# Kernel optimization log

Hardware: AMD Instinct MI355X
Metric: run time of the kernel (lower is better)

## Reference

```python
import jax, jax.numpy as jnp
import numpy as np
from jax import lax

C = 64
KS = 3  # filter_ks for dynamic kernel conv


def conv2d(x, w, pad, b=None):
    out = lax.conv_general_dilated(x, w, (1, 1), [(pad, pad), (pad, pad)],
                                   dimension_numbers=("NCHW", "OIHW", "NCHW"))
    if b is not None:
        out = out + b.reshape(1, -1, 1, 1)
    return out


def kernel_conv2d(feat, kernel):
    # feat: [B,C,H,W]; kernel: [B,C*KS*KS,H,W] -> per-pixel per-channel 3x3 filter
    B, Cc, H, W = feat.shape
    pad = (KS - 1) // 2
    xp = jnp.pad(feat, ((0, 0), (0, 0), (pad, pad), (pad, pad)), mode="edge")
    # patches: [B,C,KS*KS,H,W]
    patches = jnp.stack([xp[:, :, i:i + H, j:j + W]
                         for i in range(KS) for j in range(KS)], axis=2)
    K = kernel.reshape(B, Cc, KS * KS, H, W)
    return jnp.sum(patches * K, axis=2)


def setup_inputs() -> dict:
    key = jax.random.key(0)
    ks = jax.random.split(key, 24)
    B, H, W = 8, 128, 128
    s = lambda *sh: 1.0 / np.sqrt(np.prod(sh[1:]))
    def w(k, *sh):
        return jax.random.normal(k, sh, dtype=jnp.float32) * s(*sh)
    return {
        "f_event": jax.random.normal(ks[0], (B, C, H, W), dtype=jnp.float32),
        "f_blur": jax.random.normal(ks[1], (B, C, H, W), dtype=jnp.float32),
        # trans: conv3x3 -> ReLU -> conv3x3 (no bias)
        "Wt1": w(ks[2], C, C, 3, 3), "Wt2": w(ks[3], C, C, 3, 3),
        # trans2: conv3x3 -> ReLU
        "Wt3": w(ks[4], C, C, 3, 3),
        # F_mlp: Linear(C,2C) -> ReLU -> Linear(2C,C) -> Sigmoid
        "A1": w(ks[5], 2 * C, C), "b1": jnp.zeros((2 * C,), jnp.float32),
        "A2": w(ks[6], C, 2 * C), "b2": jnp.zeros((C,), jnp.float32),
        # gernerate_kernel: conv3x3(bias) -> ReLU -> conv1x1(bias) to C*KS^2
        "G1": w(ks[7], C, C, 3, 3), "g1b": jnp.zeros((C,), jnp.float32),
        "G2": w(ks[8], C * KS * KS, C, 1, 1), "g2b": jnp.zeros((C * KS * KS,), jnp.float32),
        # gate_rgb: conv1x1 C->1, bias
        "Rw": w(ks[9], 1, C, 1, 1), "rb": jnp.zeros((1,), jnp.float32),
        # body_sa: conv3x3 -> ReLU -> conv3x3 (no bias)
        "S1": w(ks[10], C, C, 3, 3), "S2": w(ks[11], C, C, 3, 3),
        # spatial_e: BasicConv(2,1,5,pad=2,relu=False), bias
        "Ew": w(ks[12], 1, 2, 5, 5), "eb": jnp.zeros((1,), jnp.float32),
        # conv1x1_fusion: 2C->2C, no bias
        "Fw": w(ks[13], 2 * C, 2 * C, 1, 1),
    }


def reference(f_event, f_blur, Wt1, Wt2, Wt3, A1, b1, A2, b2,
              G1, g1b, G2, g2b, Rw, rb, S1, S2, Ew, eb, Fw):
    fused = f_event + f_blur
    fused = conv2d(jax.nn.relu(conv2d(fused, Wt1, 1)), Wt2, 1)  # trans
    # SE-style channel gate
    w0 = jnp.mean(fused, axis=(2, 3))                      # [B,C]
    w0 = jax.nn.relu(w0 @ A1.T + b1)
    w0 = jax.nn.sigmoid(w0 @ A2.T + b2)                    # [B,C]
    f_b = f_blur + w0[:, :, None, None] * f_blur
    fused2 = fused + jax.nn.relu(conv2d(fused, Wt3, 1))    # trans2 + residual
    rgb_att = conv2d(fused2, Rw, 0, rb)                    # [B,1,H,W]
    f_b = f_b + rgb_att * f_b
    # dynamic per-pixel kernel from events
    kern = conv2d(jax.nn.relu(conv2d(f_event, G1, 1, g1b)), G2, 0, g2b)
    f_b = f_b + kernel_conv2d(f_b, kern)
    # spatial attention on events
    sa = conv2d(jax.nn.relu(conv2d(f_event, S1, 1)), S2, 1)
    comp = jnp.concatenate([jnp.max(sa, axis=1, keepdims=True),
                            jnp.mean(sa, axis=1, keepdims=True)], axis=1)
    scale_e = jax.nn.sigmoid(conv2d(comp, Ew, 2, eb))      # [B,1,H,W]
    f_e = f_event + scale_e * f_event
    res = conv2d(jnp.concatenate([f_e, f_b], axis=1), Fw, 0)
    return res
```

## Files before the change

kernel.cpp:

```cpp
#include <hip/hip_runtime.h>
#include <math.h>

constexpr int Bn = 8, Cn = 64, Hn = 128, Wn = 128;
constexpr int HW  = Hn * Wn;
constexpr int CHW = Cn * HW;
constexpr size_t NB = (size_t)Bn * CHW;

typedef float  f32x4  __attribute__((ext_vector_type(4)));
typedef __bf16 bf16x8 __attribute__((ext_vector_type(8)));
typedef unsigned int u32x4 __attribute__((ext_vector_type(4)));
typedef unsigned int u32x2 __attribute__((ext_vector_type(2)));

static __device__ __forceinline__ unsigned short f2bf(float f) {
    unsigned u = __builtin_bit_cast(unsigned, f);
    u = (u + 0x7FFF + ((u >> 16) & 1)) >> 16;
    return (unsigned short)u;
}
static __device__ __forceinline__ float bf2f(unsigned short v) {
    unsigned u = (unsigned)v << 16;
    return __builtin_bit_cast(float, u);
}
static __device__ __forceinline__ float bfhalf(unsigned u, int hi) {
    unsigned r = hi ? (u & 0xffff0000u) : (u << 16);
    return __builtin_bit_cast(float, r);
}

__global__ void prep_w_k(const float* __restrict__ W0, const float* __restrict__ W1,
                         const float* __restrict__ W2, const float* __restrict__ W3,
                         const float* __restrict__ W4, const float* __restrict__ W5,
                         unsigned short* __restrict__ dst) {
    int i = blockIdx.x * 256 + threadIdx.x;
    if (i >= 36864) return;
    const float* W = W0;
    switch (blockIdx.y) {
        case 1: W = W1; break; case 2: W = W2; break;
        case 3: W = W3; break; case 4: W = W4; break; case 5: W = W5; break;
        default: break;
    }
    int cj = i & 7;
    int rest = i >> 3;
    int co = rest & 63;
    rest >>= 6;
    int t  = rest % 9;
    int hs = rest / 9;
    int ci = hs * 8 + cj;
    dst[(size_t)blockIdx.y * 36864 + i] = f2bf(W[(co * 64 + ci) * 9 + t]);
}

__global__ void prep2_k(const float* __restrict__ G2, const float* __restrict__ Fw,
                        unsigned short* __restrict__ G2p, unsigned short* __restrict__ Fwp) {
    int i = blockIdx.x * 256 + threadIdx.x;
    if (i < 36864) G2p[i] = f2bf(G2[i]);
    else if (i < 36864 + 16384) Fwp[i - 36864] = f2bf(Fw[i - 36864]);
}

__global__ void pre_blk_k(const float* __restrict__ fe, const float* __restrict__ fb,
                          unsigned short* __restrict__ evb, unsigned short* __restrict__ f0b,
                          unsigned short* __restrict__ fbb) {
    int i = blockIdx.x * 256 + threadIdx.x;
    int px = i & 16383;
    int oct = (i >> 14) & 7;
    int b = i >> 17;
    const float* pe = fe + (size_t)b * CHW + (size_t)oct * 8 * HW + px;
    const float* pb = fb + (size_t)b * CHW + (size_t)oct * 8 * HW + px;
    u32x4 ev, f0, fbv;
#pragma unroll
    for (int q = 0; q < 4; ++q) {
        float e0 = pe[(size_t)(2 * q) * HW],     b0 = pb[(size_t)(2 * q) * HW];
        float e1 = pe[(size_t)(2 * q + 1) * HW], b1 = pb[(size_t)(2 * q + 1) * HW];
        ev[q]  = (unsigned)f2bf(e0) | ((unsigned)f2bf(e1) << 16);
        f0[q]  = (unsigned)f2bf(e0 + b0) | ((unsigned)f2bf(e1 + b1) << 16);
        fbv[q] = (unsigned)f2bf(b0) | ((unsigned)f2bf(b1) << 16);
    }
    const size_t o = ((size_t)(b * 8 + oct) * HW + px) * 8;
    *(u32x4*)(evb + o) = ev;
    *(u32x4*)(f0b + o) = f0;
    *(u32x4*)(fbb + o) = fbv;
}

template<bool RELU, bool BIAS, bool ADD_INPUT, bool RGB, bool COMP, bool STORE>
__global__ __launch_bounds__(256, 3) void conv3x3_blk(
        const unsigned short* __restrict__ in, const unsigned short* __restrict__ Wg,
        const float* __restrict__ bias, unsigned short* __restrict__ out,
        const float* __restrict__ gw, const float* __restrict__ gb,
        float* __restrict__ gout) {
    __shared__ unsigned short smIn[20736];
    const int b  = blockIdx.z;
    const int by = blockIdx.y << 4, bx = blockIdx.x << 4;
    const int tid = threadIdx.x;
    const int lane = tid & 63, w = tid >> 6;
    const int lx = lane & 15, ls = lane >> 4;

    for (int idx = tid; idx < 2592; idx += 256) {
        int oct = idx / 324;
        int p   = idx - oct * 324;
        int yy = p / 18, xx = p - yy * 18;
        int gy = by + yy - 1, gx = bx + xx - 1;
        u32x4 v = u32x4{0u, 0u, 0u, 0u};
        if ((unsigned)gy < (unsigned)Hn && (unsigned)gx < (unsigned)Wn)
            v = *(const u32x4*)(in + ((size_t)(b * 8 + oct) * HW + gy * Wn + gx) * 8);
        *(u32x4*)(smIn + idx * 8) = v;
    }
    __syncthreads();

    f32x4 acc[4][4];
#pragma unroll
    for (int m = 0; m < 4; ++m)
#pragma unroll
        for (int n = 0; n < 4; ++n) acc[m][n] = f32x4{0.f, 0.f, 0.f, 0.f};

#pragma unroll
    for (int ky = 0; ky < 3; ++ky)
#pragma unroll
    for (int kx = 0; kx < 3; ++kx) {
        const int t = ky * 3 + kx;
#pragma unroll
        for (int kk = 0; kk < 2; ++kk) {
            bf16x8 a[4];
            const unsigned short* wbase = Wg + kk * 18432 + ls * 4608 + t * 512 + lx * 8;
#pragma unroll
            for (int m = 0; m < 4; ++m)
                a[m] = *(const bf16x8*)(wbase + m * 128);
            const unsigned short* ibase =
                smIn + ((kk * 4 + ls) * 324 + (4 * w + ky) * 18 + lx + kx) * 8;
#pragma unroll
            for (int n = 0; n < 4; ++n) {
                bf16x8 bf = *(const bf16x8*)(ibase + n * 144);
#pragma unroll
                for (int m = 0; m < 4; ++m)
                    acc[m][n] = __builtin_amdgcn_mfma_f32_16x16x32_bf16(
                        a[m], bf, acc[m][n], 0, 0, 0);
            }
        }
    }

    const int y0 = by + 4 * w;
    float gs[4], gm[4];
    if constexpr (RGB || COMP) {
#pragma unroll
        for (int n = 0; n < 4; ++n) { gs[n] = 0.f; gm[n] = -1e30f; }
    }
#pragma unroll
    for (int m = 0; m < 4; ++m) {
        float4 rw4;
        if constexpr (RGB) rw4 = *(const float4*)(gw + 16 * m + ls * 4);
        const float rwf[4] = {RGB ? rw4.x : 0.f, RGB ? rw4.y : 0.f,
                              RGB ? rw4.z : 0.f, RGB ? rw4.w : 0.f};
        float bv[4] = {0.f, 0.f, 0.f, 0.f};
        if constexpr (BIAS) {
            float4 b4 = *(const float4*)(bias + 16 * m + ls * 4);
            bv[0] = b4.x; bv[1] = b4.y; bv[2] = b4.z; bv[3] = b4.w;
        }
        const size_t rowb = (size_t)(b * 8 + m * 2 + (ls >> 1)) * HW;
        const int j0 = (ls & 1) * 4;
#pragma unroll
        for (int n = 0; n < 4; ++n) {
            const size_t pofs = rowb + (size_t)(y0 + n) * Wn + bx + lx;
            u32x2 rin;
            if constexpr (ADD_INPUT) rin = *(const u32x2*)(in + pofs * 8 + j0);
            float vr[4];
#pragma unroll
            for (int r = 0; r < 4; ++r) {
                float v = acc[m][n][r] + bv[r];
                if constexpr (RELU) v = fmaxf(v, 0.f);
                if constexpr (ADD_INPUT) v += bfhalf(rin[r >> 1], r & 1);
                vr[r] = v;
                if constexpr (RGB) gs[n] = fmaf(rwf[r], v, gs[n]);
                if constexpr (COMP) { gm[n] = fmaxf(gm[n], v); gs[n] += v; }
            }
            if constexpr (STORE) {
                u32x2 pk;
                pk[0] = (unsigned)f2bf(vr[0]) | ((unsigned)f2bf(vr[1]) << 16);
                pk[1] = (unsigned)f2bf(vr[2]) | ((unsigned)f2bf(vr[3]) << 16);
                *(u32x2*)(out + pofs * 8 + j0) = pk;
            }
        }
    }
    if constexpr (RGB) {
#pragma unroll
        for (int n = 0; n < 4; ++n) {
            float s = gs[n];
            s += __shfl_xor(s, 16);
            s += __shfl_xor(s, 32);
            if (ls == 0)
                gout[(size_t)b * HW + (size_t)(y0 + n) * Wn + bx + lx] = s + gb[0];
        }
    }
    if constexpr (COMP) {
#pragma unroll
        for (int n = 0; n < 4; ++n) {
            float s = gs[n], mx = gm[n];
            s += __shfl_xor(s, 16);
            s += __shfl_xor(s, 32);
            mx = fmaxf(mx, __shfl_xor(mx, 16));
            mx = fmaxf(mx, __shfl_xor(mx, 32));
            if (ls == 0) {
                const size_t o = (size_t)b * 2 * HW + (size_t)(y0 + n) * Wn + bx + lx;
                gout[o]      = mx;
                gout[o + HW] = s * (1.f / 64.f);
            }
        }
    }
}

__global__ __launch_bounds__(256, 3) void conv3x3_l1_blk(
        const unsigned short* __restrict__ f0, const unsigned short* __restrict__ ev,
        const unsigned short* __restrict__ Wt1g, const unsigned short* __restrict__ G1g,
        const unsigned short* __restrict__ S1g, const float* __restrict__ g1b,
        unsigned short* __restrict__ out_t1, unsigned short* __restrict__ out_h,
        unsigned short* __restrict__ out_s1) {
    __shared__ unsigned short smIn[20736];
    const int z = blockIdx.z;
    const int b = z & 7, sel = z >> 3;
    const unsigned short* in = (sel == 0) ? f0 : ev;
    const unsigned short* Wg = (sel == 0) ? Wt1g : ((sel == 1) ? G1g : S1g);
    unsigned short* out = (sel == 0) ? out_t1 : ((sel == 1) ? out_h : out_s1);
    const int by = blockIdx.y << 4, bx = blockIdx.x << 4;
    const int tid = threadIdx.x;
    const int lane = tid & 63, w = tid >> 6;
    const int lx = lane & 15, ls = lane >> 4;

    for (int idx = tid; idx < 2592; idx += 256) {
        int oct = idx / 324;
        int p   = idx - oct * 324;
        int yy = p / 18, xx = p - yy * 18;
        int gy = by + yy - 1, gx = bx + xx - 1;
        u32x4 v = u32x4{0u, 0u, 0u, 0u};
        if ((unsigned)gy < (unsigned)Hn && (unsigned)gx < (unsigned)Wn)
            v = *(const u32x4*)(in + ((size_t)(b * 8 + oct) * HW + gy * Wn + gx) * 8);
        *(u32x4*)(smIn + idx * 8) = v;
    }
    __syncthreads();

    f32x4 acc[4][4];
#pragma unroll
    for (int m = 0; m < 4; ++m)
#pragma unroll
        for (int n = 0; n < 4; ++n) acc[m][n] = f32x4{0.f, 0.f, 0.f, 0.f};

#pragma unroll
    for (int ky = 0; ky < 3; ++ky)
#pragma unroll
    for (int kx = 0; kx < 3; ++kx) {
        const int t = ky * 3 + kx;
#pragma unroll
        for (int kk = 0; kk < 2; ++kk) {
            bf16x8 a[4];
            const unsigned short* wbase = Wg + kk * 18432 + ls * 4608 + t * 512 + lx * 8;
#pragma unroll
            for (int m = 0; m < 4; ++m)
                a[m] = *(const bf16x8*)(wbase + m * 128);
            const unsigned short* ibase =
                smIn + ((kk * 4 + ls) * 324 + (4 * w + ky) * 18 + lx + kx) * 8;
#pragma unroll
            for (int n = 0; n < 4; ++n) {
                bf16x8 bf = *(const bf16x8*)(ibase + n * 144);
#pragma unroll
                for (int m = 0; m < 4; ++m)
                    acc[m][n] = __builtin_amdgcn_mfma_f32_16x16x32_bf16(
                        a[m], bf, acc[m][n], 0, 0, 0);
            }
        }
    }

    const int y0 = by + 4 * w;
#pragma unroll
    for (int m = 0; m < 4; ++m) {
        float bv[4] = {0.f, 0.f, 0.f, 0.f};
        if (sel == 1) {
            float4 b4 = *(const float4*)(g1b + 16 * m + ls * 4);
            bv[0] = b4.x; bv[1] = b4.y; bv[2] = b4.z; bv[3] = b4.w;
        }
        const size_t rowb = (size_t)(b * 8 + m * 2 + (ls >> 1)) * HW;
        const int j0 = (ls & 1) * 4;
#pragma unroll
        for (int n = 0; n < 4; ++n) {
            const size_t pofs = rowb + (size_t)(y0 + n) * Wn + bx + lx;
            float vr[4];
#pragma unroll
            for (int r = 0; r < 4; ++r)
                vr[r] = fmaxf(acc[m][n][r] + bv[r], 0.f);
            u32x2 pk;
            pk[0] = (unsigned)f2bf(vr[0]) | ((unsigned)f2bf(vr[1]) << 16);
            pk[1] = (unsigned)f2bf(vr[2]) | ((unsigned)f2bf(vr[3]) << 16);
            *(u32x2*)(out + pofs * 8 + j0) = pk;
        }
    }
}

__global__ __launch_bounds__(256, 3) void conv3x3_l2_blk(
        const unsigned short* __restrict__ t1, const unsigned short* __restrict__ s1,
        const unsigned short* __restrict__ Wt2g, const unsigned short* __restrict__ S2g,
        unsigned short* __restrict__ out_f, float* __restrict__ comp) {
    __shared__ unsigned short smIn[20736];
    const int z = blockIdx.z;
    const int b = z & 7, sel = z >> 3;
    const unsigned short* in = (sel == 0) ? t1 : s1;
    const unsigned short* Wg = (sel == 0) ? Wt2g : S2g;
    const int by = blockIdx.y << 4, bx = blockIdx.x << 4;
    const int tid = threadIdx.x;
    const int lane = tid & 63, w = tid >> 6;
    const int lx = lane & 15, ls = lane >> 4;

    for (int idx = tid; idx < 2592; idx += 256) {
        int oct = idx / 324;
        int p   = idx - oct * 324;
        int yy = p / 18, xx = p - yy * 18;
        int gy = by + yy - 1, gx = bx + xx - 1;
        u32x4 v = u32x4{0u, 0u, 0u, 0u};
        if ((unsigned)gy < (unsigned)Hn && (unsigned)gx < (unsigned)Wn)
            v = *(const u32x4*)(in + ((size_t)(b * 8 + oct) * HW + gy * Wn + gx) * 8);
        *(u32x4*)(smIn + idx * 8) = v;
    }
    __syncthreads();

    f32x4 acc[4][4];
#pragma unroll
    for (int m = 0; m < 4; ++m)
#pragma unroll
        for (int n = 0; n < 4; ++n) acc[m][n] = f32x4{0.f, 0.f, 0.f, 0.f};

#pragma unroll
    for (int ky = 0; ky < 3; ++ky)
#pragma unroll
    for (int kx = 0; kx < 3; ++kx) {
        const int t = ky * 3 + kx;
#pragma unroll
        for (int kk = 0; kk < 2; ++kk) {
            bf16x8 a[4];
            const unsigned short* wbase = Wg + kk * 18432 + ls * 4608 + t * 512 + lx * 8;
#pragma unroll
            for (int m = 0; m < 4; ++m)
                a[m] = *(const bf16x8*)(wbase + m * 128);
            const unsigned short* ibase =
                smIn + ((kk * 4 + ls) * 324 + (4 * w + ky) * 18 + lx + kx) * 8;
#pragma unroll
            for (int n = 0; n < 4; ++n) {
                bf16x8 bf = *(const bf16x8*)(ibase + n * 144);
#pragma unroll
                for (int m = 0; m < 4; ++m)
                    acc[m][n] = __builtin_amdgcn_mfma_f32_16x16x32_bf16(
                        a[m], bf, acc[m][n], 0, 0, 0);
            }
        }
    }

    const int y0 = by + 4 * w;
    if (sel == 0) {
#pragma unroll
        for (int m = 0; m < 4; ++m) {
            const size_t rowb = (size_t)(b * 8 + m * 2 + (ls >> 1)) * HW;
            const int j0 = (ls & 1) * 4;
#pragma unroll
            for (int n = 0; n < 4; ++n) {
                const size_t pofs = rowb + (size_t)(y0 + n) * Wn + bx + lx;
                u32x2 pk;
                pk[0] = (unsigned)f2bf(acc[m][n][0]) | ((unsigned)f2bf(acc[m][n][1]) << 16);
                pk[1] = (unsigned)f2bf(acc[m][n][2]) | ((unsigned)f2bf(acc[m][n][3]) << 16);
                *(u32x2*)(out_f + pofs * 8 + j0) = pk;
            }
        }
    } else {
        float gs[4], gm[4];
#pragma unroll
        for (int n = 0; n < 4; ++n) { gs[n] = 0.f; gm[n] = -1e30f; }
#pragma unroll
        for (int m = 0; m < 4; ++m)
#pragma unroll
            for (int r = 0; r < 4; ++r)
#pragma unroll
                for (int n = 0; n < 4; ++n) {
                    float v = acc[m][n][r];
                    gm[n] = fmaxf(gm[n], v);
                    gs[n] += v;
                }
#pragma unroll
        for (int n = 0; n < 4; ++n) {
            float s = gs[n], mx = gm[n];
            s += __shfl_xor(s, 16);
            s += __shfl_xor(s, 32);
            mx = fmaxf(mx, __shfl_xor(mx, 16));
            mx = fmaxf(mx, __shfl_xor(mx, 32));
            if (ls == 0) {
                const size_t o = (size_t)b * 2 * HW + (size_t)(y0 + n) * Wn + bx + lx;
                comp[o]      = mx;
                comp[o + HW] = s * (1.f / 64.f);
            }
        }
    }
}

__global__ void mean_hw_blk(const unsigned short* __restrict__ in, float* __restrict__ w0) {
    __shared__ float red[256][8];
    const int bo = blockIdx.x;
    const int tid = threadIdx.x;
    const unsigned short* p = in + (size_t)bo * HW * 8;
    float s[8];
#pragma unroll
    for (int j = 0; j < 8; ++j) s[j] = 0.f;
    for (int it = 0; it < 64; ++it) {
        u32x4 v = *(const u32x4*)(p + (size_t)(tid + it * 256) * 8);
#pragma unroll
        for (int j = 0; j < 8; ++j) s[j] += bfhalf(v[j >> 1], j & 1);
    }
#pragma unroll
    for (int j = 0; j < 8; ++j) red[tid][j] = s[j];
    __syncthreads();
    for (int off = 128; off > 0; off >>= 1) {
        if (tid < off)
#pragma unroll
            for (int j = 0; j < 8; ++j) red[tid][j] += red[tid + off][j];
        __syncthreads();
    }
    if (tid < 8) w0[bo * 8 + tid] = red[0][tid] * (1.f / 16384.f);
}

__global__ void mlp_k(const float* __restrict__ w0, const float* __restrict__ A1,
                      const float* __restrict__ b1, const float* __restrict__ A2,
                      const float* __restrict__ b2, float* __restrict__ w0s) {
    int b = blockIdx.x, t = threadIdx.x;
    __shared__ float w0r[64], hid[128];
    if (t < 64) w0r[t] = w0[b * 64 + t];
    __syncthreads();
    float s = b1[t];
    for (int c = 0; c < 64; ++c) s = fmaf(A1[t * 64 + c], w0r[c], s);
    hid[t] = fmaxf(s, 0.f);
    __syncthreads();
    if (t < 64) {
        float s2 = b2[t];
        for (int j = 0; j < 128; ++j) s2 = fmaf(A2[t * 128 + j], hid[j], s2);
        w0s[b * 64 + t] = 1.f / (1.f + expf(-s2));
    }
}

__global__ __launch_bounds__(256, 4) void dynfused_k(
        const unsigned short* __restrict__ fbb, const unsigned short* __restrict__ hb,
        const unsigned short* __restrict__ G2p, const float* __restrict__ g2b,
        const float* __restrict__ w0s, const float* __restrict__ rgb,
        unsigned short* __restrict__ outb) {
    __shared__ unsigned short smU[8192];
    __shared__ unsigned short smFB[11520];
    const int b  = blockIdx.z;
    const int by = blockIdx.y << 3, bx = blockIdx.x << 4;
    const int tid = threadIdx.x;
    const int lane = tid & 63, w = tid >> 6;
    const int lx = lane & 15, ls = lane >> 4;
    const int wr = w & 1, wc = w >> 1;
    const int px = tid & 127;
    const int chalf = __builtin_amdgcn_readfirstlane(tid >> 7);
    const int ty = px >> 4, tx = px & 15;

#pragma unroll
    for (int it = 0; it < 4; ++it) {
        int i = tid + it * 256;
        int p = i & 127, oct = i >> 7;
        const unsigned short* sp =
            hb + ((size_t)(b * 8 + oct) * HW + (by + (p >> 4)) * Wn + bx + (p & 15)) * 8;
        ((u32x4*)smU)[oct * 128 + p] = *(const u32x4*)sp;
    }
    const float* rgbb = rgb + (size_t)b * HW;
    for (int i = tid; i < 1440; i += 256) {
        int oct = i / 180, p = i - oct * 180;
        int pr = p / 18, pc = p - pr * 18;
        int gy = min(max(by + pr - 1, 0), Hn - 1);
        int gx = min(max(bx + pc - 1, 0), Wn - 1);
        u32x4 v = *(const u32x4*)(fbb + ((size_t)(b * 8 + oct) * HW + gy * Wn + gx) * 8);
        float g = 1.f + rgbb[gy * Wn + gx];
        float4 s0 = *(const float4*)(w0s + b * 64 + oct * 8);
        float4 s1 = *(const float4*)(w0s + b * 64 + oct * 8 + 4);
        const float sc[8] = {1.f + s0.x, 1.f + s0.y, 1.f + s0.z, 1.f + s0.w,
                             1.f + s1.x, 1.f + s1.y, 1.f + s1.z, 1.f + s1.w};
#pragma unroll
        for (int j = 0; j < 8; ++j)
            smFB[(oct * 8 + j) * 180 + p] = f2bf(bfhalf(v[j >> 1], j & 1) * sc[j] * g);
    }
    __syncthreads();

    bf16x8 bv[2][4];
#pragma unroll
    for (int kk = 0; kk < 2; ++kk)
#pragma unroll
        for (int n = 0; n < 4; ++n)
            bv[kk][n] = *(const bf16x8*)(smU + ((kk * 4 + ls) * 128 + wc * 64 + n * 16 + lx) * 8);
    __syncthreads();

    float acc[32];
#pragma unroll
    for (int s = 0; s < 32; ++s) acc[s] = 0.f;

#pragma unroll
    for (int chunk = 0; chunk < 9; ++chunk) {
        f32x4 ka[2][4];
#pragma unroll
        for (int m = 0; m < 2; ++m)
#pragma unroll
            for (int n = 0; n < 4; ++n) ka[m][n] = f32x4{0.f, 0.f, 0.f, 0.f};
#pragma unroll
        for (int kk = 0; kk < 2; ++kk) {
            bf16x8 a[2];
#pragma unroll
            for (int m = 0; m < 2; ++m)
                a[m] = *(const bf16x8*)(G2p +
                        (size_t)(chunk * 64 + wr * 32 + m * 16 + lx) * 64 + kk * 32 + ls * 8);
#pragma unroll
            for (int n = 0; n < 4; ++n)
#pragma unroll
                for (int m = 0; m < 2; ++m)
                    ka[m][n] = __builtin_amdgcn_mfma_f32_16x16x32_bf16(a[m], bv[kk][n], ka[m][n], 0, 0, 0);
        }
#pragma unroll
        for (int m = 0; m < 2; ++m) {
            const float4 bb4 = *(const float4*)(g2b + chunk * 64 + wr * 32 + m * 16 + ls * 4);
            const float bb[4] = {bb4.x, bb4.y, bb4.z, bb4.w};
            const int rl0 = wr * 32 + m * 16 + ls * 4;
            const int gr = rl0 >> 3, sub = rl0 & 7;
#pragma unroll
            for (int n = 0; n < 4; ++n) {
                const int pxl = wc * 64 + n * 16 + lx;
                u32x2 pk;
                pk[0] = (unsigned)f2bf(ka[m][n][0] + bb[0]) |
                        ((unsigned)f2bf(ka[m][n][1] + bb[1]) << 16);
                pk[1] = (unsigned)f2bf(ka[m][n][2] + bb[2]) |
                        ((unsigned)f2bf(ka[m][n][3] + bb[3]) << 16);
                *(u32x2*)(smU + pxl * 64 + ((gr ^ (pxl & 7)) << 3) + sub) = pk;
            }
        }
        __syncthreads();
        u32x4 kvr[8];
#pragma unroll
        for (int k = 0; k < 8; ++k)
            kvr[k] = *(const u32x4*)(smU + px * 64 + ((k ^ (px & 7)) << 3));
#pragma unroll
        for (int rl = 0; rl < 64; ++rl) {
            const int r = chunk * 64 + rl;
            const int c = r / 9, t = r - c * 9;
            const int s = c >> 1;
            if ((c & 1) == chalf) {
                float kv = bfhalf(kvr[rl >> 3][(rl & 7) >> 1], rl & 1);
                float pv = bf2f(smFB[c * 180 + (ty + t / 3) * 18 + tx + (t % 3)]);
                acc[s] = fmaf(kv, pv, acc[s]);
            }
        }
        __syncthreads();
    }

#pragma unroll
    for (int s = 0; s < 32; ++s) {
        const int c = 2 * s + chalf;
        float res = bf2f(smFB[c * 180 + (ty + 1) * 18 + (tx + 1)]);
        smU[c * 128 + px] = f2bf(acc[s] + res);
    }
    __syncthreads();
#pragma unroll
    for (int it = 0; it < 4; ++it) {
        int i = tid + it * 256;
        int p = i & 127, oct = i >> 7;
        u32x4 pk;
#pragma unroll
        for (int q = 0; q < 4; ++q)
            pk[q] = (unsigned)smU[(oct * 8 + 2 * q) * 128 + p] |
                    ((unsigned)smU[(oct * 8 + 2 * q + 1) * 128 + p] << 16);
        *(u32x4*)(outb + ((size_t)(b * 8 + oct) * HW + (by + (p >> 4)) * Wn + bx + (p & 15)) * 8) = pk;
    }
}

__global__ __launch_bounds__(256, 2) void fuse_mfma_k(
        const unsigned short* __restrict__ evb, const float* __restrict__ scale,
        const unsigned short* __restrict__ fb2b, const unsigned short* __restrict__ Fwp,
        float* __restrict__ out) {
    __shared__ unsigned short smF[16384];
    const int bid = blockIdx.x;
    const int b = bid >> 7, px0 = (bid & 127) << 7;
    const int tid = threadIdx.x;
    const int lane = tid & 63, w = tid >> 6;
    const int lx = lane & 15, ls = lane >> 4;
    const int wr = w & 1, wc = w >> 1;
    const float* sc = scale + b * HW + px0;

#pragma unroll
    for (int it = 0; it < 8; ++it) {
        int slot = tid + it * 256;
        int oct = slot >> 7, pxl = slot & 127;
        u32x4 v;
        if (oct < 8) {
            v = *(const u32x4*)(evb + ((size_t)(b * 8 + oct) * HW + px0 + pxl) * 8);
            float s = 1.f + sc[pxl];
#pragma unroll
            for (int q = 0; q < 4; ++q)
                v[q] = (unsigned)f2bf(bfhalf(v[q], 0) * s) |
                       ((unsigned)f2bf(bfhalf(v[q], 1) * s) << 16);
        } else {
            v = *(const u32x4*)(fb2b + ((size_t)(b * 8 + oct - 8) * HW + px0 + pxl) * 8);
        }
        ((u32x4*)smF)[oct * 128 + pxl] = v;
    }
    __syncthreads();

    f32x4 acc[4][4];
#pragma unroll
    for (int m = 0; m < 4; ++m)
#pragma unroll
        for (int n = 0; n < 4; ++n) acc[m][n] = f32x4{0.f, 0.f, 0.f, 0.f};

#pragma unroll
    for (int kk = 0; kk < 4; ++kk) {
        bf16x8 a[4];
#pragma unroll
        for (int m = 0; m < 4; ++m)
            a[m] = *(const bf16x8*)(Fwp + (size_t)(wr * 64 + m * 16 + lx) * 128 + kk * 32 + ls * 8);
#pragma unroll
        for (int n = 0; n < 4; ++n) {
            bf16x8 bv = *(const bf16x8*)(smF + ((kk * 4 + ls) * 128 + wc * 64 + n * 16 + lx) * 8);
#pragma unroll
            for (int m = 0; m < 4; ++m)
                acc[m][n] = __builtin_amdgcn_mfma_f32_16x16x32_bf16(a[m], bv, acc[m][n], 0, 0, 0);
        }
    }

    const size_t ob = (size_t)b * 2 * CHW + px0 + wc * 64;
#pragma unroll
    for (int m = 0; m < 4; ++m)
#pragma unroll
        for (int n = 0; n < 4; ++n)
#pragma unroll
            for (int j = 0; j < 4; ++j) {
                const int co = wr * 64 + m * 16 + ls * 4 + j;
                out[ob + (size_t)co * HW + n * 16 + lx] = acc[m][n][j];
            }
}

__global__ void sconv5_k(const float* __restrict__ comp, const float* __restrict__ Ew,
                         const float* __restrict__ eb, float* __restrict__ scale) {
    int id = blockIdx.x * 256 + threadIdx.x;
    int b = id >> 14, p = id & 16383;
    int y = p >> 7, x = p & 127;
    const float* cb = comp + (size_t)b * 2 * HW;
    float acc = eb[0];
#pragma unroll
    for (int ch = 0; ch < 2; ++ch)
#pragma unroll
        for (int ky = 0; ky < 5; ++ky) {
            int gy = y + ky - 2;
            if ((unsigned)gy >= (unsigned)Hn) continue;
#pragma unroll
            for (int kx = 0; kx < 5; ++kx) {
                int gx = x + kx - 2;
                if ((unsigned)gx >= (unsigned)Wn) continue;
                acc = fmaf(Ew[ch * 25 + ky * 5 + kx], cb[ch * HW + gy * Wn + gx], acc);
            }
        }
    scale[id] = 1.f / (1.f + expf(-acc));
}

extern "C" void kernel_launch(void* const* d_in, const int* in_sizes, int n_in,
                              void* d_out, int out_size, void* d_ws, size_t ws_size,
                              hipStream_t stream) {
    const float* f_event = (const float*)d_in[0];
    const float* f_blur  = (const float*)d_in[1];
    const float* Wt1 = (const float*)d_in[2];
    const float* Wt2 = (const float*)d_in[3];
    const float* Wt3 = (const float*)d_in[4];
    const float* A1  = (const float*)d_in[5];
    const float* b1  = (const float*)d_in[6];
    const float* A2  = (const float*)d_in[7];
    const float* b2  = (const float*)d_in[8];
    const float* G1  = (const float*)d_in[9];
    const float* g1b = (const float*)d_in[10];
    const float* G2  = (const float*)d_in[11];
    const float* g2b = (const float*)d_in[12];
    const float* Rw  = (const float*)d_in[13];
    const float* rb  = (const float*)d_in[14];
    const float* S1  = (const float*)d_in[15];
    const float* S2  = (const float*)d_in[16];
    const float* Ew  = (const float*)d_in[17];
    const float* eb  = (const float*)d_in[18];
    const float* Fw  = (const float*)d_in[19];
    float* out = (float*)d_out;

    float* ws    = (float*)d_ws;
    float* w0    = ws;
    float* w0s   = w0 + 512;
    float* rgb   = w0s + 512;
    float* comp  = rgb + Bn * HW;
    float* scale = comp + 2 * Bn * HW;
    unsigned short* wprep = (unsigned short*)(scale + Bn * HW);
    unsigned short* G2p = wprep + 6 * 36864;
    unsigned short* Fwp = G2p + 36864;
    unsigned short* B0 = Fwp + 16384;
    unsigned short* B1 = B0 + NB;
    unsigned short* B2 = B1 + NB;
    unsigned short* B3 = B2 + NB;
    unsigned short* B4 = B3 + NB;
    unsigned short* B5 = B4 + NB;
    unsigned short* B6 = B5 + NB;

    prep_w_k<<<dim3(144, 6), 256, 0, stream>>>(Wt1, Wt2, Wt3, G1, S1, S2, wprep);
    prep2_k<<<208, 256, 0, stream>>>(G2, Fw, G2p, Fwp);
    pre_blk_k<<<4096, 256, 0, stream>>>(f_event, f_blur, B0, B1, B5);
    conv3x3_l1_blk<<<dim3(8, 8, 24), 256, 0, stream>>>(
        B1, B0, wprep + 0 * 36864, wprep + 3 * 36864, wprep + 4 * 36864, g1b,
        B2, B4, B6);
    conv3x3_l2_blk<<<dim3(8, 8, 16), 256, 0, stream>>>(
        B2, B6, wprep + 1 * 36864, wprep + 5 * 36864, B3, comp);
    mean_hw_blk<<<Bn * 8, 256, 0, stream>>>(B3, w0);
    mlp_k<<<Bn, 128, 0, stream>>>(w0, A1, b1, A2, b2, w0s);
    sconv5_k<<<Bn * HW / 256, 256, 0, stream>>>(comp, Ew, eb, scale);
    conv3x3_blk<true, false, true, true, false, false><<<dim3(8, 8, Bn), 256, 0, stream>>>(
        B3, wprep + 2 * 36864, nullptr, nullptr, Rw, rb, rgb);
    dynfused_k<<<dim3(8, 16, Bn), 256, 0, stream>>>(B5, B4, G2p, g2b, w0s, rgb, B3);
    fuse_mfma_k<<<Bn * HW / 128, 256, 0, stream>>>(B0, scale, B3, Fwp, out);
}
```

Before: 222.3 us.

## Use direct global-to-LDS loads and merge spatial conv into rgb kernel

Replaces register-staged global-to-shared copies of conv input halos with the global_load_lds builtin, pointing out-of-bounds halo lanes at a zeroed pad buffer. The 5x5 spatial-attention conv kernel is folded into the rgb gate conv launch as extra z-blocks, removing one launch and letting both run concurrently. fuse_mfma_k raises its occupancy hint and loads the fb2 half directly into LDS. The direct-LDS path depends on builtin availability and on correct synchronisation with asynchronous LDS writes.

```diff
diff --git a/kernel.cpp b/kernel.cpp
--- a/kernel.cpp
+++ b/kernel.cpp
@@ -23,6 +23,16 @@
 static __device__ __forceinline__ float bfhalf(unsigned u, int hi) {
     unsigned r = hi ? (u & 0xffff0000u) : (u << 16);
     return __builtin_bit_cast(float, r);
+}
+
+static __device__ __forceinline__ void gl_lds16(const unsigned short* g, unsigned short* l) {
+#if defined(__has_builtin) && __has_builtin(__builtin_amdgcn_global_load_lds)
+    __builtin_amdgcn_global_load_lds(
+        (const __attribute__((address_space(1))) void*)g,
+        (__attribute__((address_space(3))) void*)l, 16, 0, 0);
+#else
+    *(u32x4*)l = *(const u32x4*)g;
+#endif
 }
 
 __global__ void prep_w_k(const float* __restrict__ W0, const float* __restrict__ W1,
@@ -48,8 +58,10 @@
 }
 
 __global__ void prep2_k(const float* __restrict__ G2, const float* __restrict__ Fw,
-                        unsigned short* __restrict__ G2p, unsigned short* __restrict__ Fwp) {
+                        unsigned short* __restrict__ G2p, unsigned short* __restrict__ Fwp,
+                        unsigned short* __restrict__ zp) {
     int i = blockIdx.x * 256 + threadIdx.x;
+    if (i < 64) zp[i] = 0;
     if (i < 36864) G2p[i] = f2bf(G2[i]);
     else if (i < 36864 + 16384) Fwp[i - 36864] = f2bf(Fw[i - 36864]);
 }
@@ -78,137 +90,12 @@
     *(u32x4*)(fbb + o) = fbv;
 }
 
-template<bool RELU, bool BIAS, bool ADD_INPUT, bool RGB, bool COMP, bool STORE>
-__global__ __launch_bounds__(256, 3) void conv3x3_blk(
-        const unsigned short* __restrict__ in, const unsigned short* __restrict__ Wg,
-        const float* __restrict__ bias, unsigned short* __restrict__ out,
-        const float* __restrict__ gw, const float* __restrict__ gb,
-        float* __restrict__ gout) {
-    __shared__ unsigned short smIn[20736];
-    const int b  = blockIdx.z;
-    const int by = blockIdx.y << 4, bx = blockIdx.x << 4;
-    const int tid = threadIdx.x;
-    const int lane = tid & 63, w = tid >> 6;
-    const int lx = lane & 15, ls = lane >> 4;
-
-    for (int idx = tid; idx < 2592; idx += 256) {
-        int oct = idx / 324;
-        int p   = idx - oct * 324;
-        int yy = p / 18, xx = p - yy * 18;
-        int gy = by + yy - 1, gx = bx + xx - 1;
-        u32x4 v = u32x4{0u, 0u, 0u, 0u};
-        if ((unsigned)gy < (unsigned)Hn && (unsigned)gx < (unsigned)Wn)
-            v = *(const u32x4*)(in + ((size_t)(b * 8 + oct) * HW + gy * Wn + gx) * 8);
-        *(u32x4*)(smIn + idx * 8) = v;
-    }
-    __syncthreads();
-
-    f32x4 acc[4][4];
-#pragma unroll
-    for (int m = 0; m < 4; ++m)
-#pragma unroll
-        for (int n = 0; n < 4; ++n) acc[m][n] = f32x4{0.f, 0.f, 0.f, 0.f};
-
-#pragma unroll
-    for (int ky = 0; ky < 3; ++ky)
-#pragma unroll
-    for (int kx = 0; kx < 3; ++kx) {
-        const int t = ky * 3 + kx;
-#pragma unroll
-        for (int kk = 0; kk < 2; ++kk) {
-            bf16x8 a[4];
-            const unsigned short* wbase = Wg + kk * 18432 + ls * 4608 + t * 512 + lx * 8;
-#pragma unroll
-            for (int m = 0; m < 4; ++m)
-                a[m] = *(const bf16x8*)(wbase + m * 128);
-            const unsigned short* ibase =
-                smIn + ((kk * 4 + ls) * 324 + (4 * w + ky) * 18 + lx + kx) * 8;
-#pragma unroll
-            for (int n = 0; n < 4; ++n) {
-                bf16x8 bf = *(const bf16x8*)(ibase + n * 144);
-#pragma unroll
-                for (int m = 0; m < 4; ++m)
-                    acc[m][n] = __builtin_amdgcn_mfma_f32_16x16x32_bf16(
-                        a[m], bf, acc[m][n], 0, 0, 0);
-            }
-        }
-    }
-
-    const int y0 = by + 4 * w;
-    float gs[4], gm[4];
-    if constexpr (RGB || COMP) {
-#pragma unroll
-        for (int n = 0; n < 4; ++n) { gs[n] = 0.f; gm[n] = -1e30f; }
-    }
-#pragma unroll
-    for (int m = 0; m < 4; ++m) {
-        float4 rw4;
-        if constexpr (RGB) rw4 = *(const float4*)(gw + 16 * m + ls * 4);
-        const float rwf[4] = {RGB ? rw4.x : 0.f, RGB ? rw4.y : 0.f,
-                              RGB ? rw4.z : 0.f, RGB ? rw4.w : 0.f};
-        float bv[4] = {0.f, 0.f, 0.f, 0.f};
-        if constexpr (BIAS) {
-            float4 b4 = *(const float4*)(bias + 16 * m + ls * 4);
-            bv[0] = b4.x; bv[1] = b4.y; bv[2] = b4.z; bv[3] = b4.w;
-        }
-        const size_t rowb = (size_t)(b * 8 + m * 2 + (ls >> 1)) * HW;
-        const int j0 = (ls & 1) * 4;
-#pragma unroll
-        for (int n = 0; n < 4; ++n) {
-            const size_t pofs = rowb + (size_t)(y0 + n) * Wn + bx + lx;
-            u32x2 rin;
-            if constexpr (ADD_INPUT) rin = *(const u32x2*)(in + pofs * 8 + j0);
-            float vr[4];
-#pragma unroll
-            for (int r = 0; r < 4; ++r) {
-                float v = acc[m][n][r] + bv[r];
-                if constexpr (RELU) v = fmaxf(v, 0.f);
-                if constexpr (ADD_INPUT) v += bfhalf(rin[r >> 1], r & 1);
-                vr[r] = v;
-                if constexpr (RGB) gs[n] = fmaf(rwf[r], v, gs[n]);
-                if constexpr (COMP) { gm[n] = fmaxf(gm[n], v); gs[n] += v; }
-            }
-            if constexpr (STORE) {
-                u32x2 pk;
-                pk[0] = (unsigned)f2bf(vr[0]) | ((unsigned)f2bf(vr[1]) << 16);
-                pk[1] = (unsigned)f2bf(vr[2]) | ((unsigned)f2bf(vr[3]) << 16);
-                *(u32x2*)(out + pofs * 8 + j0) = pk;
-            }
-        }
-    }
-    if constexpr (RGB) {
-#pragma unroll
-        for (int n = 0; n < 4; ++n) {
-            float s = gs[n];
-            s += __shfl_xor(s, 16);
-            s += __shfl_xor(s, 32);
-            if (ls == 0)
-                gout[(size_t)b * HW + (size_t)(y0 + n) * Wn + bx + lx] = s + gb[0];
-        }
-    }
-    if constexpr (COMP) {
-#pragma unroll
-        for (int n = 0; n < 4; ++n) {
-            float s = gs[n], mx = gm[n];
-            s += __shfl_xor(s, 16);
-            s += __shfl_xor(s, 32);
-            mx = fmaxf(mx, __shfl_xor(mx, 16));
-            mx = fmaxf(mx, __shfl_xor(mx, 32));
-            if (ls == 0) {
-                const size_t o = (size_t)b * 2 * HW + (size_t)(y0 + n) * Wn + bx + lx;
-                gout[o]      = mx;
-                gout[o + HW] = s * (1.f / 64.f);
-            }
-        }
-    }
-}
-
 __global__ __launch_bounds__(256, 3) void conv3x3_l1_blk(
         const unsigned short* __restrict__ f0, const unsigned short* __restrict__ ev,
         const unsigned short* __restrict__ Wt1g, const unsigned short* __restrict__ G1g,
         const unsigned short* __restrict__ S1g, const float* __restrict__ g1b,
         unsigned short* __restrict__ out_t1, unsigned short* __restrict__ out_h,
-        unsigned short* __restrict__ out_s1) {
+        unsigned short* __restrict__ out_s1, const unsigned short* __restrict__ zp) {
     __shared__ unsigned short smIn[20736];
     const int z = blockIdx.z;
     const int b = z & 7, sel = z >> 3;
@@ -225,10 +112,10 @@
         int p   = idx - oct * 324;
         int yy = p / 18, xx = p - yy * 18;
         int gy = by + yy - 1, gx = bx + xx - 1;
-        u32x4 v = u32x4{0u, 0u, 0u, 0u};
-        if ((unsigned)gy < (unsigned)Hn && (unsigned)gx < (unsigned)Wn)
-            v = *(const u32x4*)(in + ((size_t)(b * 8 + oct) * HW + gy * Wn + gx) * 8);
-        *(u32x4*)(smIn + idx * 8) = v;
+        const unsigned short* src =
+            ((unsigned)gy < (unsigned)Hn && (unsigned)gx < (unsigned)Wn)
+            ? in + ((size_t)(b * 8 + oct) * HW + gy * Wn + gx) * 8 : zp;
+        gl_lds16(src, smIn + idx * 8);
     }
     __syncthreads();
 
@@ -291,7 +178,8 @@
 __global__ __launch_bounds__(256, 3) void conv3x3_l2_blk(
         const unsigned short* __restrict__ t1, const unsigned short* __restrict__ s1,
         const unsigned short* __restrict__ Wt2g, const unsigned short* __restrict__ S2g,
-        unsigned short* __restrict__ out_f, float* __restrict__ comp) {
+        unsigned short* __restrict__ out_f, float* __restrict__ comp,
+        const unsigned short* __restrict__ zp) {
     __shared__ unsigned short smIn[20736];
     const int z = blockIdx.z;
     const int b = z & 7, sel = z >> 3;
@@ -307,10 +195,10 @@
         int p   = idx - oct * 324;
         int yy = p / 18, xx = p - yy * 18;
         int gy = by + yy - 1, gx = bx + xx - 1;
-        u32x4 v = u32x4{0u, 0u, 0u, 0u};
-        if ((unsigned)gy < (unsigned)Hn && (unsigned)gx < (unsigned)Wn)
-            v = *(const u32x4*)(in + ((size_t)(b * 8 + oct) * HW + gy * Wn + gx) * 8);
-        *(u32x4*)(smIn + idx * 8) = v;
+        const unsigned short* src =
+            ((unsigned)gy < (unsigned)Hn && (unsigned)gx < (unsigned)Wn)
+            ? in + ((size_t)(b * 8 + oct) * HW + gy * Wn + gx) * 8 : zp;
+        gl_lds16(src, smIn + idx * 8);
     }
     __syncthreads();
 
@@ -387,6 +275,117 @@
                 comp[o + HW] = s * (1.f / 64.f);
             }
         }
+    }
+}
+
+__global__ __launch_bounds__(256, 3) void rgb_sconv_k(
+        const unsigned short* __restrict__ in, const unsigned short* __restrict__ Wg,
+        const float* __restrict__ gw, const float* __restrict__ gb,
+        float* __restrict__ gout,
+        const float* __restrict__ comp, const float* __restrict__ Ew,
+        const float* __restrict__ eb, float* __restrict__ scale,
+        const unsigned short* __restrict__ zp) {
+    __shared__ unsigned short smIn[20736];
+    const int z = blockIdx.z;
+    if (z >= 8) {
+        int id = (((z - 8) * 64) + blockIdx.y * 8 + blockIdx.x) * 256 + threadIdx.x;
+        int sb = id >> 14, p = id & 16383;
+        int y = p >> 7, x = p & 127;
+        const float* cb = comp + (size_t)sb * 2 * HW;
+        float sacc = eb[0];
+#pragma unroll
+        for (int ch = 0; ch < 2; ++ch)
+#pragma unroll
+            for (int ky = 0; ky < 5; ++ky) {
+                int gy = y + ky - 2;
+                if ((unsigned)gy >= (unsigned)Hn) continue;
+#pragma unroll
+                for (int kx = 0; kx < 5; ++kx) {
+                    int gx = x + kx - 2;
+                    if ((unsigned)gx >= (unsigned)Wn) continue;
+                    sacc = fmaf(Ew[ch * 25 + ky * 5 + kx], cb[ch * HW + gy * Wn + gx], sacc);
+                }
+            }
+        scale[id] = 1.f / (1.f + expf(-sacc));
+        return;
+    }
+    const int b = z;
+    const int by = blockIdx.y << 4, bx = blockIdx.x << 4;
+    const int tid = threadIdx.x;
+    const int lane = tid & 63, w = tid >> 6;
+    const int lx = lane & 15, ls = lane >> 4;
+
+    for (int idx = tid; idx < 2592; idx += 256) {
+        int oct = idx / 324;
+        int p   = idx - oct * 324;
+        int yy = p / 18, xx = p - yy * 18;
+        int gy = by + yy - 1, gx = bx + xx - 1;
+        const unsigned short* src =
+            ((unsigned)gy < (unsigned)Hn && (unsigned)gx < (unsigned)Wn)
+            ? in + ((size_t)(b * 8 + oct) * HW + gy * Wn + gx) * 8 : zp;
+        gl_lds16(src, smIn + idx * 8);
+    }
+    __syncthreads();
+
+    f32x4 acc[4][4];
+#pragma unroll
+    for (int m = 0; m < 4; ++m)
+#pragma unroll
+        for (int n = 0; n < 4; ++n) acc[m][n] = f32x4{0.f, 0.f, 0.f, 0.f};
+
+#pragma unroll
+    for (int ky = 0; ky < 3; ++ky)
+#pragma unroll
+    for (int kx = 0; kx < 3; ++kx) {
+        const int t = ky * 3 + kx;
+#pragma unroll
+        for (int kk = 0; kk < 2; ++kk) {
+            bf16x8 a[4];
+            const unsigned short* wbase = Wg + kk * 18432 + ls * 4608 + t * 512 + lx * 8;
+#pragma unroll
+            for (int m = 0; m < 4; ++m)
+                a[m] = *(const bf16x8*)(wbase + m * 128);
+            const unsigned short* ibase =
+                smIn + ((kk * 4 + ls) * 324 + (4 * w + ky) * 18 + lx + kx) * 8;
+#pragma unroll
+            for (int n = 0; n < 4; ++n) {
+                bf16x8 bf = *(const bf16x8*)(ibase + n * 144);
+#pragma unroll
+                for (int m = 0; m < 4; ++m)
+                    acc[m][n] = __builtin_amdgcn_mfma_f32_16x16x32_bf16(
+                        a[m], bf, acc[m][n], 0, 0, 0);
+            }
+        }
+    }
+
+    const int y0 = by + 4 * w;
+    float gs[4];
+#pragma unroll
+    for (int n = 0; n < 4; ++n) gs[n] = 0.f;
+#pragma unroll
+    for (int m = 0; m < 4; ++m) {
+        float4 rw4 = *(const float4*)(gw + 16 * m + ls * 4);
+        const float rwf[4] = {rw4.x, rw4.y, rw4.z, rw4.w};
+        const size_t rowb = (size_t)(b * 8 + m * 2 + (ls >> 1)) * HW;
+        const int j0 = (ls & 1) * 4;
+#pragma unroll
+        for (int n = 0; n < 4; ++n) {
+            const size_t pofs = rowb + (size_t)(y0 + n) * Wn + bx + lx;
+            u32x2 rin = *(const u32x2*)(in + pofs * 8 + j0);
+#pragma unroll
+            for (int r = 0; r < 4; ++r) {
+                float v = fmaxf(acc[m][n][r], 0.f) + bfhalf(rin[r >> 1], r & 1);
+                gs[n] = fmaf(rwf[r], v, gs[n]);
+            }
+        }
+    }
+#pragma unroll
+    for (int n = 0; n < 4; ++n) {
+        float s = gs[n];
+        s += __shfl_xor(s, 16);
+        s += __shfl_xor(s, 32);
+        if (ls == 0)
+            gout[(size_t)b * HW + (size_t)(y0 + n) * Wn + bx + lx] = s + gb[0];
     }
 }
 
@@ -454,9 +453,8 @@
     for (int it = 0; it < 4; ++it) {
         int i = tid + it * 256;
         int p = i & 127, oct = i >> 7;
-        const unsigned short* sp =
-            hb + ((size_t)(b * 8 + oct) * HW + (by + (p >> 4)) * Wn + bx + (p & 15)) * 8;
-        ((u32x4*)smU)[oct * 128 + p] = *(const u32x4*)sp;
+        gl_lds16(hb + ((size_t)(b * 8 + oct) * HW + (by + (p >> 4)) * Wn + bx + (p & 15)) * 8,
+                 smU + i * 8);
     }
     const float* rgbb = rgb + (size_t)b * HW;
     for (int i = tid; i < 1440; i += 256) {
@@ -564,7 +562,7 @@
     }
 }
 
-__global__ __launch_bounds__(256, 2) void fuse_mfma_k(
+__global__ __launch_bounds__(256, 3) void fuse_mfma_k(
         const unsigned short* __restrict__ evb, const float* __restrict__ scale,
         const unsigned short* __restrict__ fb2b, const unsigned short* __restrict__ Fwp,
         float* __restrict__ out) {
@@ -578,21 +576,22 @@
     const float* sc = scale + b * HW + px0;
 
 #pragma unroll
-    for (int it = 0; it < 8; ++it) {
+    for (int it = 4; it < 8; ++it) {
         int slot = tid + it * 256;
         int oct = slot >> 7, pxl = slot & 127;
-        u32x4 v;
-        if (oct < 8) {
-            v = *(const u32x4*)(evb + ((size_t)(b * 8 + oct) * HW + px0 + pxl) * 8);
-            float s = 1.f + sc[pxl];
-#pragma unroll
-            for (int q = 0; q < 4; ++q)
-                v[q] = (unsigned)f2bf(bfhalf(v[q], 0) * s) |
-                       ((unsigned)f2bf(bfhalf(v[q], 1) * s) << 16);
-        } else {
-            v = *(const u32x4*)(fb2b + ((size_t)(b * 8 + oct - 8) * HW + px0 + pxl) * 8);
-        }
-        ((u32x4*)smF)[oct * 128 + pxl] = v;
+        gl_lds16(fb2b + ((size_t)(b * 8 + oct - 8) * HW + px0 + pxl) * 8, smF + slot * 8);
+    }
+#pragma unroll
+    for (int it = 0; it < 4; ++it) {
+        int slot = tid + it * 256;
+        int oct = slot >> 7, pxl = slot & 127;
+        u32x4 v = *(const u32x4*)(evb + ((size_t)(b * 8 + oct) * HW + px0 + pxl) * 8);
+        float s = 1.f + sc[pxl];
+#pragma unroll
+        for (int q = 0; q < 4; ++q)
+            v[q] = (unsigned)f2bf(bfhalf(v[q], 0) * s) |
+                   ((unsigned)f2bf(bfhalf(v[q], 1) * s) << 16);
+        ((u32x4*)smF)[slot] = v;
     }
     __syncthreads();
 
@@ -627,29 +626,6 @@
                 const int co = wr * 64 + m * 16 + ls * 4 + j;
                 out[ob + (size_t)co * HW + n * 16 + lx] = acc[m][n][j];
             }
-}
-
-__global__ void sconv5_k(const float* __restrict__ comp, const float* __restrict__ Ew,
-                         const float* __restrict__ eb, float* __restrict__ scale) {
-    int id = blockIdx.x * 256 + threadIdx.x;
-    int b = id >> 14, p = id & 16383;
-    int y = p >> 7, x = p & 127;
-    const float* cb = comp + (size_t)b * 2 * HW;
-    float acc = eb[0];
-#pragma unroll
-    for (int ch = 0; ch < 2; ++ch)
-#pragma unroll
-        for (int ky = 0; ky < 5; ++ky) {
-            int gy = y + ky - 2;
-            if ((unsigned)gy >= (unsigned)Hn) continue;
-#pragma unroll
-            for (int kx = 0; kx < 5; ++kx) {
-                int gx = x + kx - 2;
-                if ((unsigned)gx >= (unsigned)Wn) continue;
-                acc = fmaf(Ew[ch * 25 + ky * 5 + kx], cb[ch * HW + gy * Wn + gx], acc);
-            }
-        }
-    scale[id] = 1.f / (1.f + expf(-acc));
 }
 
 extern "C" void kernel_launch(void* const* d_in, const int* in_sizes, int n_in,
@@ -686,7 +662,8 @@
     unsigned short* wprep = (unsigned short*)(scale + Bn * HW);
     unsigned short* G2p = wprep + 6 * 36864;
     unsigned short* Fwp = G2p + 36864;
-    unsigned short* B0 = Fwp + 16384;
+    unsigned short* zpad = Fwp + 16384;
+    unsigned short* B0 = zpad + 64;
     unsigned short* B1 = B0 + NB;
     unsigned short* B2 = B1 + NB;
     unsigned short* B3 = B2 + NB;
@@ -695,18 +672,17 @@
     unsigned short* B6 = B5 + NB;
 
     prep_w_k<<<dim3(144, 6), 256, 0, stream>>>(Wt1, Wt2, Wt3, G1, S1, S2, wprep);
-    prep2_k<<<208, 256, 0, stream>>>(G2, Fw, G2p, Fwp);
+    prep2_k<<<208, 256, 0, stream>>>(G2, Fw, G2p, Fwp, zpad);
     pre_blk_k<<<4096, 256, 0, stream>>>(f_event, f_blur, B0, B1, B5);
     conv3x3_l1_blk<<<dim3(8, 8, 24), 256, 0, stream>>>(
         B1, B0, wprep + 0 * 36864, wprep + 3 * 36864, wprep + 4 * 36864, g1b,
-        B2, B4, B6);
+        B2, B4, B6, zpad);
     conv3x3_l2_blk<<<dim3(8, 8, 16), 256, 0, stream>>>(
-        B2, B6, wprep + 1 * 36864, wprep + 5 * 36864, B3, comp);
+        B2, B6, wprep + 1 * 36864, wprep + 5 * 36864, B3, comp, zpad);
     mean_hw_blk<<<Bn * 8, 256, 0, stream>>>(B3, w0);
     mlp_k<<<Bn, 128, 0, stream>>>(w0, A1, b1, A2, b2, w0s);
-    sconv5_k<<<Bn * HW / 256, 256, 0, stream>>>(comp, Ew, eb, scale);
-    conv3x3_blk<true, false, true, true, false, false><<<dim3(8, 8, Bn), 256, 0, stream>>>(
-        B3, wprep + 2 * 36864, nullptr, nullptr, Rw, rb, rgb);
+    rgb_sconv_k<<<dim3(8, 8, 16), 256, 0, stream>>>(
+        B3, wprep + 2 * 36864, Rw, rb, rgb, comp, Ew, eb, scale, zpad);
     dynfused_k<<<dim3(8, 16, Bn), 256, 0, stream>>>(B5, B4, G2p, g2b, w0s, rgb, B3);
     fuse_mfma_k<<<Bn * HW / 128, 256, 0, stream>>>(B0, scale, B3, Fwp, out);
 }
```

After: 220.8 us (median of 2 runs). About the same (-0.7%).
